# Kernel optimization log

Hardware: AMD Instinct MI355X
Metric: run time of the kernel (lower is better)

Reference implementation:

```python
import jax, jax.numpy as jnp
import numpy as np

EPS = 1e-5

def _layernorm(x, w, b):
    mu = jnp.mean(x, axis=-1, keepdims=True)
    var = jnp.mean(jnp.square(x - mu), axis=-1, keepdims=True)
    return (x - mu) * jax.lax.rsqrt(var + EPS) * w + b

def setup_inputs() -> dict:
    key = jax.random.key(0)
    ks = jax.random.split(key, 8)
    B, N, D = 1, 512, 128
    x = jax.random.normal(ks[0], (B, N, N, D), dtype=jnp.float32)
    mask = jnp.ones((B, N, N), dtype=jnp.float32)
    # learned params (torch nn.Linear stores weight as (out, in))
    p_in_w = jax.random.normal(ks[1], (2 * D, D), dtype=jnp.float32) * (1.0 / np.sqrt(D))
    g_in_w = jax.random.normal(ks[2], (2 * D, D), dtype=jnp.float32) * 0.02
    p_out_w = jax.random.normal(ks[3], (D, D), dtype=jnp.float32) * 0.02
    g_out_w = jax.random.normal(ks[4], (D, D), dtype=jnp.float32) * 0.02
    norm_in_w = jnp.ones((D,), dtype=jnp.float32)
    norm_in_b = jnp.zeros((D,), dtype=jnp.float32)
    norm_out_w = jnp.ones((D,), dtype=jnp.float32)
    norm_out_b = jnp.zeros((D,), dtype=jnp.float32)
    return {"x": x, "mask": mask, "norm_in_w": norm_in_w, "norm_in_b": norm_in_b,
            "p_in_w": p_in_w, "g_in_w": g_in_w, "norm_out_w": norm_out_w,
            "norm_out_b": norm_out_b, "p_out_w": p_out_w, "g_out_w": g_out_w}

def reference(x, mask, norm_in_w, norm_in_b, p_in_w, g_in_w, norm_out_w, norm_out_b, p_out_w, g_out_w):
    # x: (B,N,N,D), mask: (B,N,N)
    x_ln = _layernorm(x, norm_in_w, norm_in_b)          # (B,N,N,D)
    x_in = x_ln
    # gated dual projection to 2D channels, then mask
    h = jnp.einsum('bijd,ed->bije', x_ln, p_in_w) * jax.nn.sigmoid(
        jnp.einsum('bijd,ed->bije', x_ln, g_in_w))      # (B,N,N,2D)
    h = h * mask[..., None]
    D = x.shape[-1]
    a, b = h[..., :D], h[..., D:]                        # (B,N,N,D) each
    # triangular 'outgoing' contraction over k
    t = jnp.einsum('bikd,bjkd->bijd', a, b)              # (B,N,N,D)
    out = jnp.einsum('bijd,ed->bije', _layernorm(t, norm_out_w, norm_out_b), p_out_w) \
        * jax.nn.sigmoid(jnp.einsum('bijd,ed->bije', x_in, g_out_w))
    return out
```

## Files before the change

### kernel.cpp

```cpp
#include <hip/hip_runtime.h>
#include <stdint.h>

#define NSEQ 512
#define DDIM 128
#define NROWS (NSEQ * NSEQ)
#define PMASK (NROWS - 1)
#define ROT(idx, d) (((idx) + (d) * 128) & PMASK)

typedef __bf16 bf16x8 __attribute__((ext_vector_type(8)));
typedef __bf16 bf16x2v __attribute__((ext_vector_type(2)));
typedef unsigned short u16;
typedef u16 ushort8 __attribute__((ext_vector_type(8)));
typedef float f32x4 __attribute__((ext_vector_type(4)));
typedef uint32_t u32x4 __attribute__((ext_vector_type(4)));
typedef uint32_t u32x2 __attribute__((ext_vector_type(2)));

__device__ __forceinline__ u16 cvt1(float f) {
  return __builtin_bit_cast(u16, (__bf16)f);
}
__device__ __forceinline__ uint32_t pk2(float a, float b) {
  bf16x2v v = {(__bf16)a, (__bf16)b};
  return __builtin_bit_cast(uint32_t, v);
}
__device__ __forceinline__ float bf2f(u16 u) {
  uint32_t x = ((uint32_t)u) << 16;
  return __builtin_bit_cast(float, x);
}
__device__ __forceinline__ f32x4 mfma_bf16(ushort8 a, ushort8 b, f32x4 c) {
  return __builtin_amdgcn_mfma_f32_16x16x32_bf16(
      __builtin_bit_cast(bf16x8, a), __builtin_bit_cast(bf16x8, b), c, 0, 0, 0);
}
__device__ __forceinline__ float sigmoidf_(float x) {
  return __builtin_amdgcn_rcpf(1.0f + __expf(-x));
}

#define ROR16(v, n)                                                            \
  __builtin_bit_cast(float, __builtin_amdgcn_update_dpp(                       \
      __builtin_bit_cast(int, (v)), __builtin_bit_cast(int, (v)),              \
      0x120 + (n), 0xF, 0xF, false))

#define GLOAD16(gp, lp)                                                        \
  __builtin_amdgcn_global_load_lds(                                            \
      (const __attribute__((address_space(1))) void*)(gp),                     \
      (__attribute__((address_space(3))) void*)(lp), 16, 0, 0)

__global__ __launch_bounds__(256) void k0_prep(
    const float* __restrict__ p_in_w, const float* __restrict__ g_in_w,
    const float* __restrict__ p_out_w, const float* __restrict__ g_out_w,
    const float* __restrict__ now, const float* __restrict__ nob,
    u16* __restrict__ Wb, u16* __restrict__ Pb, u16* __restrict__ Gb,
    float* __restrict__ S12) {
  const int b = blockIdx.x, t = threadIdx.x;
#pragma unroll
  for (int k = 0; k < 2; ++k) {
    const int idx = b * 512 + k * 256 + t;
    const float v = (idx < 32768) ? p_in_w[idx] : g_in_w[idx - 32768];
    Wb[idx] = cvt1(v);
  }
  if (t < 128) {
    const int idx = b * 128 + t;
    const int d = idx & 127;
    Pb[idx] = cvt1(p_out_w[idx] * now[d]);
    Gb[idx] = cvt1(g_out_w[idx]);
  }
  const int w = t >> 6, lane = t & 63;
  if (w >= 2) {
    const float* wv = (w == 2) ? now : nob;
    float p = p_out_w[b * 128 + lane] * wv[lane] +
              p_out_w[b * 128 + 64 + lane] * wv[64 + lane];
#pragma unroll
    for (int m = 1; m < 64; m <<= 1) p += __shfl_xor(p, m);
    if (lane == 0) S12[2 * b + (w - 2)] = p;
  }
}

__global__ __launch_bounds__(256, 4) void k1_ln_proj(
    const float* __restrict__ x, const float* __restrict__ mask,
    const float* __restrict__ niw, const float* __restrict__ nib,
    const u16* __restrict__ Wb, const u16* __restrict__ Gb,
    u16* __restrict__ AtB, u16* __restrict__ gArg) {
  __shared__ __align__(16) u16 xln[64 * 128];
  __shared__ __align__(16) u16 stage[128 * 64];
  const int tid = threadIdx.x;
  const int lane = tid & 63;
  const int w = tid >> 6;
  const int bid = blockIdx.x;
  const int rb = (bid >> 4) * 8 + (bid & 7);
  const int cg = (bid >> 3) & 1;
  const int r0 = rb * 64;
  const int g = lane >> 4, c = lane & 15;

  f32x4 v0[4], v1[4];
#pragma unroll
  for (int it = 0; it < 4; ++it) {
    const int rl = w * 16 + it * 4 + g;
    const float* xr = x + (size_t)(r0 + rl) * DDIM + c * 8;
    v0[it] = *(const f32x4*)xr;
    v1[it] = *(const f32x4*)(xr + 4);
  }
  const f32x4 w0 = *(const f32x4*)(niw + c * 8);
  const f32x4 w1 = *(const f32x4*)(niw + c * 8 + 4);
  const f32x4 b0 = *(const f32x4*)(nib + c * 8);
  const f32x4 b1 = *(const f32x4*)(nib + c * 8 + 4);
#pragma unroll
  for (int it = 0; it < 4; ++it) {
    const int rl = w * 16 + it * 4 + g;
    float s = v0[it][0] + v0[it][1] + v0[it][2] + v0[it][3] +
              v1[it][0] + v1[it][1] + v1[it][2] + v1[it][3];
    float ss = v0[it][0] * v0[it][0] + v0[it][1] * v0[it][1] +
               v0[it][2] * v0[it][2] + v0[it][3] * v0[it][3] +
               v1[it][0] * v1[it][0] + v1[it][1] * v1[it][1] +
               v1[it][2] * v1[it][2] + v1[it][3] * v1[it][3];
    { float t1 = ROR16(s, 1); s += t1; t1 = ROR16(ss, 1); ss += t1; }
    { float t1 = ROR16(s, 2); s += t1; t1 = ROR16(ss, 2); ss += t1; }
    { float t1 = ROR16(s, 4); s += t1; t1 = ROR16(ss, 4); ss += t1; }
    { float t1 = ROR16(s, 8); s += t1; t1 = ROR16(ss, 8); ss += t1; }
    const float mu = s * (1.0f / 128.0f);
    const float rs = rsqrtf(ss * (1.0f / 128.0f) - mu * mu + 1e-5f);
    float f0 = (v0[it][0] - mu) * rs * w0[0] + b0[0];
    float f1 = (v0[it][1] - mu) * rs * w0[1] + b0[1];
    float f2 = (v0[it][2] - mu) * rs * w0[2] + b0[2];
    float f3 = (v0[it][3] - mu) * rs * w0[3] + b0[3];
    float f4 = (v1[it][0] - mu) * rs * w1[0] + b1[0];
    float f5 = (v1[it][1] - mu) * rs * w1[1] + b1[1];
    float f6 = (v1[it][2] - mu) * rs * w1[2] + b1[2];
    float f7 = (v1[it][3] - mu) * rs * w1[3] + b1[3];
    u32x4 ov{pk2(f0, f1), pk2(f2, f3), pk2(f4, f5), pk2(f6, f7)};
    const int byteoff = rl * 256 + ((c ^ (rl & 7)) << 4);
    *(u32x4*)((char*)xln + byteoff) = ov;
  }
  __syncthreads();

  const int lr = lane & 15, lq = lane >> 4;
  const int eP = cg * 128 + w * 32;
  f32x4 accP[4][2], accG[4][2];
#pragma unroll
  for (int m = 0; m < 4; ++m)
#pragma unroll
    for (int n = 0; n < 2; ++n) {
      accP[m][n] = f32x4{0.f, 0.f, 0.f, 0.f};
      accG[m][n] = f32x4{0.f, 0.f, 0.f, 0.f};
    }
#pragma unroll
  for (int ks = 0; ks < 4; ++ks) {
    const int kblk = ks * 4 + lq;
    ushort8 af[4];
#pragma unroll
    for (int m = 0; m < 4; ++m) {
      const int row = m * 16 + lr;
      af[m] = *(const ushort8*)((const char*)xln + row * 256 +
                                ((kblk ^ (row & 7)) << 4));
    }
    ushort8 bP[2], bG[2];
#pragma unroll
    for (int n = 0; n < 2; ++n) {
      const int e = eP + n * 16 + lr;
      const int dd = ks * 32 + lq * 8;
      bP[n] = *(const ushort8*)(Wb + e * 128 + dd);
      bG[n] = *(const ushort8*)(Wb + (256 + e) * 128 + dd);
    }
#pragma unroll
    for (int m = 0; m < 4; ++m)
#pragma unroll
      for (int n = 0; n < 2; ++n) {
        accP[m][n] = mfma_bf16(af[m], bP[n], accP[m][n]);
        accG[m][n] = mfma_bf16(af[m], bG[n], accG[m][n]);
      }
  }

#pragma unroll
  for (int m = 0; m < 4; ++m) {
    const int rloc = m * 16 + lq * 4;
    const f32x4 mv = *(const f32x4*)(mask + r0 + rloc);
#pragma unroll
    for (int n = 0; n < 2; ++n) {
      const int dloc = w * 32 + n * 16 + lr;
      const float o0 = accP[m][n][0] * sigmoidf_(accG[m][n][0]) * mv[0];
      const float o1 = accP[m][n][1] * sigmoidf_(accG[m][n][1]) * mv[1];
      const float o2 = accP[m][n][2] * sigmoidf_(accG[m][n][2]) * mv[2];
      const float o3 = accP[m][n][3] * sigmoidf_(accG[m][n][3]) * mv[3];
      u32x2 pk;
      pk[0] = pk2(o0, o1);
      pk[1] = pk2(o2, o3);
      const int gsw = (m * 4 + lq) ^ (dloc & 15);
      *(u32x2*)((char*)stage + dloc * 128 + (gsw << 3)) = pk;
    }
  }
  __syncthreads();

  {
    const int i_ = rb >> 3, kt = rb & 7;
    u16* dst = AtB + (((size_t)kt * 512 + i_) * 256 + cg * 128) * 64;
#pragma unroll
    for (int q = 0; q < 4; ++q) {
      const int e = q * 32 + (tid >> 3);
      const int g0 = (tid & 7) * 2;
      const u32x2 lo =
          *(const u32x2*)((const char*)stage + e * 128 + ((g0 ^ (e & 15)) << 3));
      const u32x2 hi = *(const u32x2*)((const char*)stage + e * 128 +
                                       (((g0 + 1) ^ (e & 15)) << 3));
      u32x4 outv{lo[0], lo[1], hi[0], hi[1]};
      *(u32x4*)(dst + e * 64 + (tid & 7) * 8) = outv;
    }
  }

  {
    f32x4 accO[4];
#pragma unroll
    for (int m = 0; m < 4; ++m) accO[m] = f32x4{0.f, 0.f, 0.f, 0.f};
    const int eg = cg * 64 + w * 16 + lr;
#pragma unroll
    for (int ks = 0; ks < 4; ++ks) {
      const int kblk = ks * 4 + lq;
      const ushort8 bO = *(const ushort8*)(Gb + eg * 128 + ks * 32 + lq * 8);
#pragma unroll
      for (int m = 0; m < 4; ++m) {
        const int row = m * 16 + lr;
        const ushort8 af2 = *(const ushort8*)((const char*)xln + row * 256 +
                                              ((kblk ^ (row & 7)) << 4));
        accO[m] = mfma_bf16(af2, bO, accO[m]);
      }
    }
    __syncthreads();
    u16* stage2 = stage;
    const int e_loc = w * 16 + lr;
    const int gsl = e_loc >> 2;
    const int esub = (e_loc & 3) * 2;
#pragma unroll
    for (int m = 0; m < 4; ++m) {
#pragma unroll
      for (int reg = 0; reg < 4; ++reg) {
        const int rl2 = m * 16 + lq * 4 + reg;
        *(u16*)((char*)stage2 + rl2 * 128 + ((gsl ^ (rl2 & 7)) << 3) + esub) =
            cvt1(accO[m][reg]);
      }
    }
    __syncthreads();
#pragma unroll
    for (int p = 0; p < 2; ++p) {
      const int r = p * 32 + (tid >> 3);
      const int il8 = tid & 7;
      const char* base = (const char*)stage2 + r * 128;
      const u32x2 a = *(const u32x2*)(base + (((il8 * 2) ^ (r & 7)) << 3));
      const u32x2 b = *(const u32x2*)(base + (((il8 * 2 + 1) ^ (r & 7)) << 3));
      u32x4 ov{a[0], a[1], b[0], b[1]};
      *(u32x4*)(gArg + (size_t)(r0 + r) * DDIM + cg * 64 + il8 * 8) = ov;
    }
  }
}

__global__ __launch_bounds__(256, 4) void k2_tri(const u16* __restrict__ AtB,
                                                 u16* __restrict__ Ct) {
  __shared__ __align__(16) u16 lds[16384];
  const int tid = threadIdx.x;
  const int bid = blockIdx.x;
  const int lb = (bid & 7) * 256 + (bid >> 3);
  const int d = lb >> 4;
  const int tile = lb & 15;
  const int i0 = (tile >> 2) * 128, j0 = (tile & 3) * 128;
  const int lane = tid & 63, wid = tid >> 6;
  const int wr = wid >> 1, wc = wid & 1;
  const int lr = lane & 15, lq = lane >> 4;

  f32x4 acc[4][4];
#pragma unroll
  for (int m = 0; m < 4; ++m)
#pragma unroll
    for (int n = 0; n < 4; ++n) acc[m][n] = f32x4{0.f, 0.f, 0.f, 0.f};

  for (int kt = 0; kt < 8; ++kt) {
    if (kt) __syncthreads();
#pragma unroll
    for (int q = 0; q < 4; ++q) {
      const int idx = q * 256 + tid;
      const int r = idx >> 3, bk = idx & 7;
      const int sbk = bk ^ (r & 7);
      GLOAD16(AtB + (((size_t)kt * 512 + i0 + r) * 256 + d) * 64 + sbk * 8,
              &lds[idx * 8]);
      GLOAD16(AtB + (((size_t)kt * 512 + j0 + r) * 256 + 128 + d) * 64 + sbk * 8,
              &lds[8192 + idx * 8]);
    }
    __syncthreads();

    const u16* A_l = lds;
    const u16* B_l = lds + 8192;
#pragma unroll
    for (int ks = 0; ks < 2; ++ks) {
      const int kblk = ks * 4 + lq;
      ushort8 af[4], bfr[4];
#pragma unroll
      for (int m = 0; m < 4; ++m) {
        const int row = wr * 64 + m * 16 + lr;
        af[m] = *(const ushort8*)((const char*)A_l + row * 128 +
                                  ((kblk ^ (row & 7)) << 4));
      }
#pragma unroll
      for (int n = 0; n < 4; ++n) {
        const int col = wc * 64 + n * 16 + lr;
        bfr[n] = *(const ushort8*)((const char*)B_l + col * 128 +
                                   ((kblk ^ (col & 7)) << 4));
      }
#pragma unroll
      for (int m = 0; m < 4; ++m)
#pragma unroll
        for (int n = 0; n < 4; ++n)
          acc[m][n] = mfma_bf16(af[m], bfr[n], acc[m][n]);
    }
  }

  u16* Cd = Ct + (size_t)d * NROWS;
#pragma unroll
  for (int m = 0; m < 4; ++m) {
    const int i = i0 + wr * 64 + m * 16 + lq * 4;
#pragma unroll
    for (int n = 0; n < 4; ++n) {
      const int j = j0 + wc * 64 + n * 16 + lr;
#pragma unroll
      for (int reg = 0; reg < 4; ++reg)
        Cd[ROT((i + reg) * NSEQ + j, d)] = cvt1(acc[m][n][reg]);
    }
  }
}

__global__ __launch_bounds__(256, 4) void k3_out(
    const u16* __restrict__ Ct, const u16* __restrict__ gArg,
    const u16* __restrict__ Pb, const float* __restrict__ S12,
    float* __restrict__ out) {
  __shared__ __align__(16) u16 ldsT[128 * 128];
  __shared__ float ps[4 * 128], pss[4 * 128];
  __shared__ float prm[128 * 2];
  __shared__ float s12l[128 * 2];
  const int tid = threadIdx.x, lane = tid & 63, w = tid >> 6;
  const int c0 = blockIdx.x * 128;

  {
    const int row2 = lane * 2;
    float s0 = 0.f, ss0 = 0.f, s1 = 0.f, ss1 = 0.f;
#pragma unroll
    for (int db = 0; db < 4; ++db) {
      uint32_t pe[4], po[4];
#pragma unroll
      for (int j = 0; j < 8; ++j) {
        const int d = w * 32 + db * 8 + j;
        const uint32_t v = *(const uint32_t*)(Ct + (size_t)d * NROWS +
                                              ROT(c0 + row2, d));
        const u16 ue = (u16)v, uo = (u16)(v >> 16);
        const float fe = bf2f(ue), fo = bf2f(uo);
        s0 += fe; ss0 += fe * fe;
        s1 += fo; ss1 += fo * fo;
        if (j & 1) {
          pe[j >> 1] |= ((uint32_t)ue) << 16;
          po[j >> 1] |= ((uint32_t)uo) << 16;
        } else {
          pe[j >> 1] = ue;
          po[j >> 1] = uo;
        }
      }
      const int gr = w * 4 + db;
      *(u32x4*)((char*)ldsT + row2 * 256 + ((gr ^ (row2 & 7)) << 4)) =
          u32x4{pe[0], pe[1], pe[2], pe[3]};
      *(u32x4*)((char*)ldsT + (row2 + 1) * 256 + ((gr ^ ((row2 + 1) & 7)) << 4)) =
          u32x4{po[0], po[1], po[2], po[3]};
    }
    ps[w * 128 + row2] = s0;
    pss[w * 128 + row2] = ss0;
    ps[w * 128 + row2 + 1] = s1;
    pss[w * 128 + row2 + 1] = ss1;
  }
  if (tid < 128) ((u32x2*)s12l)[tid] = ((const u32x2*)S12)[tid];
  __syncthreads();
  if (tid < 128) {
    const float s = ps[tid] + ps[128 + tid] + ps[256 + tid] + ps[384 + tid];
    const float ss = pss[tid] + pss[128 + tid] + pss[256 + tid] + pss[384 + tid];
    const float mu = s * (1.f / 128.f);
    const float rs = rsqrtf(ss * (1.f / 128.f) - mu * mu + 1e-5f);
    prm[2 * tid] = rs;
    prm[2 * tid + 1] = -rs * mu;
  }

  const int lr = lane & 15, lq = lane >> 4;
  const int rowbase = w * 32;
  f32x4 aP[2][8];
#pragma unroll
  for (int m = 0; m < 2; ++m)
#pragma unroll
    for (int n = 0; n < 8; ++n) aP[m][n] = f32x4{0.f, 0.f, 0.f, 0.f};
#pragma unroll
  for (int ks = 0; ks < 4; ++ks) {
    const int kblk = ks * 4 + lq;
    ushort8 at2[2];
#pragma unroll
    for (int m = 0; m < 2; ++m) {
      const int row = rowbase + m * 16 + lr;
      at2[m] = *(const ushort8*)((const char*)ldsT + row * 256 +
                                 ((kblk ^ (row & 7)) << 4));
    }
    ushort8 bp[8];
#pragma unroll
    for (int n = 0; n < 8; ++n) {
      const int e = n * 16 + lr;
      bp[n] = *(const ushort8*)(Pb + e * 128 + ks * 32 + lq * 8);
    }
#pragma unroll
    for (int m = 0; m < 2; ++m)
#pragma unroll
      for (int n = 0; n < 8; ++n) aP[m][n] = mfma_bf16(at2[m], bp[n], aP[m][n]);
  }
  __syncthreads();

#pragma unroll
  for (int m = 0; m < 2; ++m) {
    const int crow = rowbase + m * 16 + lq * 4;
#pragma unroll
    for (int n = 0; n < 8; ++n) {
      const int e = n * 16 + lr;
      const float s1 = s12l[2 * e], s2v = s12l[2 * e + 1];
#pragma unroll
      for (int reg = 0; reg < 4; ++reg) {
        const float rs = prm[2 * (crow + reg)];
        const float t1 = prm[2 * (crow + reg) + 1];
        const float op = rs * aP[m][n][reg] + t1 * s1 + s2v;
        const size_t r = (size_t)(c0 + crow + reg);
        const float gt = sigmoidf_(bf2f(gArg[r * DDIM + e]));
        out[r * DDIM + e] = op * gt;
      }
    }
  }
}

extern "C" void kernel_launch(void* const* d_in, const int* in_sizes, int n_in,
                              void* d_out, int out_size, void* d_ws,
                              size_t ws_size, hipStream_t stream) {
  const float* x = (const float*)d_in[0];
  const float* mask = (const float*)d_in[1];
  const float* niw = (const float*)d_in[2];
  const float* nib = (const float*)d_in[3];
  const float* p_in_w = (const float*)d_in[4];
  const float* g_in_w = (const float*)d_in[5];
  const float* now = (const float*)d_in[6];
  const float* nob = (const float*)d_in[7];
  const float* p_out_w = (const float*)d_in[8];
  const float* g_out_w = (const float*)d_in[9];
  float* out = (float*)d_out;
  char* ws = (char*)d_ws;

  u16* AtB = (u16*)(ws);
  u16* Ct = (u16*)(ws + 134217728);
  u16* gA = (u16*)(ws + 201326592);
  u16* Wb = (u16*)(ws + 268435456);
  u16* Pb = (u16*)(ws + 268566528);
  u16* Gb = (u16*)(ws + 268599296);
  float* S12 = (float*)(ws + 268632064);

  hipLaunchKernelGGL(k0_prep, dim3(128), dim3(256), 0, stream, p_in_w, g_in_w,
                     p_out_w, g_out_w, now, nob, Wb, Pb, Gb, S12);
  hipLaunchKernelGGL(k1_ln_proj, dim3(2 * NROWS / 64), dim3(256), 0, stream, x,
                     mask, niw, nib, Wb, Gb, AtB, gA);
  hipLaunchKernelGGL(k2_tri, dim3(128 * 16), dim3(256), 0, stream, AtB, Ct);
  hipLaunchKernelGGL(k3_out, dim3(NROWS / 128), dim3(256), 0, stream, Ct, gA,
                     Pb, S12, out);
}
```

Before: 311.6 us.

## Store triangle output in row-band tiled layout for contiguous k3 loads

k2 now writes the contraction result as [i][j-quarter][d][128 j] blocks instead of d-major planes with a rotation, so each k3 block reads one contiguous 32 KB chunk with 16-byte vector loads. k3 transposes into LDS with a new swizzle and computes layernorm statistics from LDS in a separate pass. The aim is to replace k3's strided 4-byte gathers across 128 d-planes with coalesced reads. In exchange, k2's scalar 2-byte stores become less coalesced, and k3 gains scalar LDS writes and an extra barrier.

```diff
diff --git a/kernel.cpp b/kernel.cpp
--- a/kernel.cpp
+++ b/kernel.cpp
@@ -4,8 +4,6 @@
 #define NSEQ 512
 #define DDIM 128
 #define NROWS (NSEQ * NSEQ)
-#define PMASK (NROWS - 1)
-#define ROT(idx, d) (((idx) + (d) * 128) & PMASK)
 
 typedef __bf16 bf16x8 __attribute__((ext_vector_type(8)));
 typedef __bf16 bf16x2v __attribute__((ext_vector_type(2)));
@@ -250,7 +248,7 @@
 }
 
 __global__ __launch_bounds__(256, 4) void k2_tri(const u16* __restrict__ AtB,
-                                                 u16* __restrict__ Ct) {
+                                                 u16* __restrict__ Ct2) {
   __shared__ __align__(16) u16 lds[16384];
   const int tid = threadIdx.x;
   const int bid = blockIdx.x;
@@ -308,70 +306,78 @@
     }
   }
 
-  u16* Cd = Ct + (size_t)d * NROWS;
+  const int jq = j0 >> 7;
 #pragma unroll
   for (int m = 0; m < 4; ++m) {
     const int i = i0 + wr * 64 + m * 16 + lq * 4;
 #pragma unroll
     for (int n = 0; n < 4; ++n) {
-      const int j = j0 + wc * 64 + n * 16 + lr;
+      const int jl = wc * 64 + n * 16 + lr;
 #pragma unroll
       for (int reg = 0; reg < 4; ++reg)
-        Cd[ROT((i + reg) * NSEQ + j, d)] = cvt1(acc[m][n][reg]);
+        Ct2[((size_t)((i + reg) * 4 + jq) * 128 + d) * 128 + jl] =
+            cvt1(acc[m][n][reg]);
     }
   }
 }
 
 __global__ __launch_bounds__(256, 4) void k3_out(
-    const u16* __restrict__ Ct, const u16* __restrict__ gArg,
+    const u16* __restrict__ Ct2, const u16* __restrict__ gArg,
     const u16* __restrict__ Pb, const float* __restrict__ S12,
     float* __restrict__ out) {
   __shared__ __align__(16) u16 ldsT[128 * 128];
-  __shared__ float ps[4 * 128], pss[4 * 128];
+  __shared__ float ps[256], pss[256];
   __shared__ float prm[128 * 2];
   __shared__ float s12l[128 * 2];
   const int tid = threadIdx.x, lane = tid & 63, w = tid >> 6;
-  const int c0 = blockIdx.x * 128;
+  const int rband = blockIdx.x;
+  const int c0 = rband * 128;
 
   {
-    const int row2 = lane * 2;
-    float s0 = 0.f, ss0 = 0.f, s1 = 0.f, ss1 = 0.f;
-#pragma unroll
-    for (int db = 0; db < 4; ++db) {
-      uint32_t pe[4], po[4];
+    const u16* src = Ct2 + (size_t)rband * 16384;
+    const int c8 = lane & 15;
+    ushort8 ch[8];
+#pragma unroll
+    for (int q = 0; q < 8; ++q) {
+      const int d = w * 32 + q * 4 + (lane >> 4);
+      ch[q] = *(const ushort8*)(src + d * 128 + c8 * 8);
+    }
+#pragma unroll
+    for (int q = 0; q < 8; ++q) {
+      const int d = w * 32 + q * 4 + (lane >> 4);
+      const int dsw = d ^ (c8 << 3);
 #pragma unroll
       for (int j = 0; j < 8; ++j) {
-        const int d = w * 32 + db * 8 + j;
-        const uint32_t v = *(const uint32_t*)(Ct + (size_t)d * NROWS +
-                                              ROT(c0 + row2, d));
-        const u16 ue = (u16)v, uo = (u16)(v >> 16);
-        const float fe = bf2f(ue), fo = bf2f(uo);
-        s0 += fe; ss0 += fe * fe;
-        s1 += fo; ss1 += fo * fo;
-        if (j & 1) {
-          pe[j >> 1] |= ((uint32_t)ue) << 16;
-          po[j >> 1] |= ((uint32_t)uo) << 16;
-        } else {
-          pe[j >> 1] = ue;
-          po[j >> 1] = uo;
-        }
-      }
-      const int gr = w * 4 + db;
-      *(u32x4*)((char*)ldsT + row2 * 256 + ((gr ^ (row2 & 7)) << 4)) =
-          u32x4{pe[0], pe[1], pe[2], pe[3]};
-      *(u32x4*)((char*)ldsT + (row2 + 1) * 256 + ((gr ^ ((row2 + 1) & 7)) << 4)) =
-          u32x4{po[0], po[1], po[2], po[3]};
-    }
-    ps[w * 128 + row2] = s0;
-    pss[w * 128 + row2] = ss0;
-    ps[w * 128 + row2 + 1] = s1;
-    pss[w * 128 + row2 + 1] = ss1;
+        const int r = c8 * 8 + j;
+        ldsT[r * 128 + dsw] = ch[q][j];
+      }
+    }
   }
   if (tid < 128) ((u32x2*)s12l)[tid] = ((const u32x2*)S12)[tid];
   __syncthreads();
+
+  {
+    const int row = tid & 127, half = tid >> 7;
+    float s = 0.f, ss = 0.f;
+#pragma unroll
+    for (int k = 0; k < 8; ++k) {
+      const int kblk = half * 8 + k;
+      const ushort8 v = *(const ushort8*)((const char*)ldsT + row * 256 +
+                                          ((kblk ^ ((row >> 3) & 15)) << 4));
+#pragma unroll
+      for (int j = 0; j < 8; ++j) {
+        const float f = bf2f(v[j]);
+        s += f;
+        ss += f * f;
+      }
+    }
+    ps[half * 128 + row] = s;
+    pss[half * 128 + row] = ss;
+  }
+  __syncthreads();
   if (tid < 128) {
-    const float s = ps[tid] + ps[128 + tid] + ps[256 + tid] + ps[384 + tid];
-    const float ss = pss[tid] + pss[128 + tid] + pss[256 + tid] + pss[384 + tid];
+    const float s = ps[tid] + ps[128 + tid];
+    const float ss = pss[tid] + pss[128 + tid];
     const float mu = s * (1.f / 128.f);
     const float rs = rsqrtf(ss * (1.f / 128.f) - mu * mu + 1e-5f);
     prm[2 * tid] = rs;
@@ -393,7 +399,7 @@
     for (int m = 0; m < 2; ++m) {
       const int row = rowbase + m * 16 + lr;
       at2[m] = *(const ushort8*)((const char*)ldsT + row * 256 +
-                                 ((kblk ^ (row & 7)) << 4));
+                                 ((kblk ^ ((row >> 3) & 15)) << 4));
     }
     ushort8 bp[8];
 #pragma unroll
@@ -445,7 +451,7 @@
   char* ws = (char*)d_ws;
 
   u16* AtB = (u16*)(ws);
-  u16* Ct = (u16*)(ws + 134217728);
+  u16* Ct2 = (u16*)(ws + 134217728);
   u16* gA = (u16*)(ws + 201326592);
   u16* Wb = (u16*)(ws + 268435456);
   u16* Pb = (u16*)(ws + 268566528);
@@ -456,7 +462,7 @@
                      p_out_w, g_out_w, now, nob, Wb, Pb, Gb, S12);
   hipLaunchKernelGGL(k1_ln_proj, dim3(2 * NROWS / 64), dim3(256), 0, stream, x,
                      mask, niw, nib, Wb, Gb, AtB, gA);
-  hipLaunchKernelGGL(k2_tri, dim3(128 * 16), dim3(256), 0, stream, AtB, Ct);
-  hipLaunchKernelGGL(k3_out, dim3(NROWS / 128), dim3(256), 0, stream, Ct, gA,
+  hipLaunchKernelGGL(k2_tri, dim3(128 * 16), dim3(256), 0, stream, AtB, Ct2);
+  hipLaunchKernelGGL(k3_out, dim3(NROWS / 128), dim3(256), 0, stream, Ct2, gA,
                      Pb, S12, out);
 }
```

Result: no change. 311.9 us (+0.1%).
